# Kernel optimization log

Hardware: AMD Instinct MI355X
Metric: run time of the kernel (lower is better)

The kernel has to match this reference:

```python
import jax, jax.numpy as jnp
import numpy as np

H = 1024
B_DIM = 64  # bottleneck
EPS = 1e-5

def setup_inputs() -> dict:
    key = jax.random.key(0)
    ks = jax.random.split(key, 5)
    x = jax.random.normal(ks[0], (8, 4096, H), dtype=jnp.float32)
    norm_w = jnp.ones((H,), jnp.float32)
    norm_b = jnp.zeros((H,), jnp.float32)
    # nn.Linear default init ~ U(-1/sqrt(fan_in), 1/sqrt(fan_in))
    lim_d = 1.0 / np.sqrt(H)
    down_w = jax.random.uniform(ks[1], (B_DIM, H), jnp.float32, -lim_d, lim_d)
    down_b = jax.random.uniform(ks[2], (B_DIM,), jnp.float32, -lim_d, lim_d)
    # NOTE: original inits up to zeros; we use small random values so the
    # computation (and gradients) are non-degenerate for kernel testing.
    lim_u = 1.0 / np.sqrt(B_DIM)
    up_w = jax.random.uniform(ks[3], (H, B_DIM), jnp.float32, -lim_u, lim_u)
    up_b = jax.random.uniform(ks[4], (H,), jnp.float32, -lim_u, lim_u)
    return {"x": x, "norm_w": norm_w, "norm_b": norm_b,
            "down_w": down_w, "down_b": down_b, "up_w": up_w, "up_b": up_b}

def reference(x, norm_w, norm_b, down_w, down_b, up_w, up_b):
    # LayerNorm over last dim, eps=1e-5 (PyTorch default)
    mu = jnp.mean(x, axis=-1, keepdims=True)
    var = jnp.mean(jnp.square(x - mu), axis=-1, keepdims=True)
    xn = (x - mu) * jax.lax.rsqrt(var + EPS) * norm_w + norm_b
    # down-proj [B,S,H] @ [H,b] -> [B,S,b]
    h = jnp.einsum('bsh,dh->bsd', xn, down_w) + down_b
    h = jax.nn.gelu(h, approximate=False)  # torch nn.GELU default = exact erf
    # up-proj [B,S,b] @ [b,H] -> [B,S,H], residual add
    out = jnp.einsum('bsd,hd->bsh', h, up_w) + up_b
    return x + out
```

## Files before the change

### kernel.cpp

```cpp
#include <hip/hip_runtime.h>


#define HDIM  1024
#define BDIM  64
#define XROWB 4112

using s16x8 = __attribute__((ext_vector_type(8))) short;
using f32x4 = __attribute__((ext_vector_type(4))) float;

__device__ float g_wstat[128];

__device__ __forceinline__ short f2bf(float f) {
  unsigned u = __builtin_bit_cast(unsigned, f);
  u += 0x7fffu + ((u >> 16) & 1u);
  return (short)(u >> 16);
}
__device__ __forceinline__ float bf2f(short s) {
  unsigned u = ((unsigned)(unsigned short)s) << 16;
  return __builtin_bit_cast(float, u);
}

__device__ __forceinline__ void gload16(const void* g, void* l) {
  __builtin_amdgcn_global_load_lds(
      (const __attribute__((address_space(1))) void*)g,
      (__attribute__((address_space(3))) void*)l,
      16, 0, 0);
}

extern "C" __global__ void prep_weights(const float* __restrict__ dw,
                                        const float* __restrict__ uw,
                                        const float* __restrict__ nw,
                                        const float* __restrict__ nb,
                                        const float* __restrict__ db,
                                        short* __restrict__ wsbf) {
  const int b = blockIdx.x;
  if (b < 64) {
    int tid = b * 256 + threadIdx.x;
    if (tid < 8192) {
      int off = tid * 8;
      int k = off & (HDIM - 1);
      f32x4 v0 = *(const f32x4*)(dw + off);
      f32x4 v1 = *(const f32x4*)(dw + off + 4);
      f32x4 g0 = *(const f32x4*)(nw + k);
      f32x4 g1 = *(const f32x4*)(nw + k + 4);
      s16x8 o;
#pragma unroll
      for (int j = 0; j < 4; ++j) {
        o[j]     = f2bf(v0[j] * g0[j]);
        o[j + 4] = f2bf(v1[j] * g1[j]);
      }
      *(s16x8*)(wsbf + tid * 8) = o;
    } else {
      int off = (tid - 8192) * 8;
      f32x4 v0 = *(const f32x4*)(uw + off);
      f32x4 v1 = *(const f32x4*)(uw + off + 4);
      s16x8 o;
#pragma unroll
      for (int j = 0; j < 4; ++j) { o[j] = f2bf(v0[j]); o[j + 4] = f2bf(v1[j]); }
      *(s16x8*)(wsbf + tid * 8) = o;
    }
  } else {
    const int t = threadIdx.x;
    const int n = t >> 2, p = t & 3;
    const float* dwn = dw + n * HDIM;
    float s1 = 0.f, s2 = 0.f;
    for (int j = 0; j < 32; ++j) {
      int k = p * 256 + j * 8;
      f32x4 v0 = *(const f32x4*)(dwn + k);
      f32x4 v1 = *(const f32x4*)(dwn + k + 4);
      f32x4 g0 = *(const f32x4*)(nw + k);
      f32x4 g1 = *(const f32x4*)(nw + k + 4);
      f32x4 b0 = *(const f32x4*)(nb + k);
      f32x4 b1 = *(const f32x4*)(nb + k + 4);
#pragma unroll
      for (int jj = 0; jj < 4; ++jj) {
        s1 += bf2f(f2bf(v0[jj] * g0[jj])) + bf2f(f2bf(v1[jj] * g1[jj]));
        s2 += v0[jj] * b0[jj] + v1[jj] * b1[jj];
      }
    }
    s1 += __shfl_xor(s1, 1); s1 += __shfl_xor(s1, 2);
    s2 += __shfl_xor(s2, 1); s2 += __shfl_xor(s2, 2);
    if (p == 0) {
      g_wstat[n]      = s1;
      g_wstat[64 + n] = db[n] + s2;
    }
  }
}

extern "C" __global__ __launch_bounds__(512, 4)
void adapter_fused(const float* __restrict__ x,
                   const float* __restrict__ ub,
                   const short* __restrict__ dwb,
                   const short* __restrict__ uwb,
                   float* __restrict__ out)
{
  __shared__ __align__(16) char  xf[16 * XROWB];
  __shared__ __align__(16) float part[2][64][20];
  __shared__ __align__(16) short g[16][72];
  __shared__ float shalf[2][16];
  __shared__ float qhalf[2][16];

  const int t    = threadIdx.x;
  const int w    = t >> 6;
  const int lane = t & 63;
  const int q    = lane >> 4;
  const int c    = lane & 15;
  const size_t rowbase = (size_t)blockIdx.x * 16;

  {
    const char* gx = (const char*)(x + rowbase * HDIM);
#pragma unroll
    for (int i = 0; i < 8; ++i) {
      const int ch = w * 8 + i;
      gload16(gx + ch * 1024 + lane * 16,
              xf + (ch >> 2) * XROWB + (ch & 3) * 1024);
    }
  }
  __syncthreads();

  {
    const int kh = w >> 2, nw = w & 3;
    const char*  arow = xf + c * XROWB + kh * 2048;
    const short* pB   = dwb + (size_t)(nw * 16 + c) * HDIM + kh * 512 + q * 8;
    f32x4 acc = {0.f, 0.f, 0.f, 0.f};
    float sum = 0.f, ssq = 0.f;
#pragma unroll
    for (int ks = 0; ks < 16; ++ks) {
      f32x4 u0 = *(const f32x4*)(arow + ks * 128 + q * 32);
      f32x4 u1 = *(const f32x4*)(arow + ks * 128 + q * 32 + 16);
      s16x8 b = *(const s16x8*)(pB + ks * 32);
      s16x8 a;
#pragma unroll
      for (int j = 0; j < 4; ++j) {
        float f0 = u0[j]; sum += f0; ssq += f0 * f0; a[j]     = f2bf(f0);
        float f1 = u1[j]; sum += f1; ssq += f1 * f1; a[j + 4] = f2bf(f1);
      }
      acc = __builtin_amdgcn_mfma_f32_16x16x32_bf16(a, b, acc, 0, 0, 0);
    }
    sum += __shfl_xor(sum, 16); sum += __shfl_xor(sum, 32);
    ssq += __shfl_xor(ssq, 16); ssq += __shfl_xor(ssq, 32);
    if (nw == 0 && lane < 16) { shalf[kh][c] = sum; qhalf[kh][c] = ssq; }
    *(f32x4*)&part[kh][nw * 16 + c][q * 4] = acc;
  }
  __syncthreads();

  if (w < 4) {
    const int n = w * 16 + c;
    f32x4 p0 = *(const f32x4*)&part[0][n][q * 4];
    f32x4 p1 = *(const f32x4*)&part[1][n][q * 4];
    f32x4 h4 = p0 + p1;
    float sT = shalf[0][c] + shalf[1][c];
    float qT = qhalf[0][c] + qhalf[1][c];
    float muv = sT * (1.0f / HDIM);
    float rsv = rsqrtf(qT * (1.0f / HDIM) - muv * muv + 1e-5f);
    const float sdw = g_wstat[n];
    const float dbv = g_wstat[64 + n];
#pragma unroll
    for (int i = 0; i < 4; ++i) {
      const float m  = __shfl(muv, q * 4 + i);
      const float rv = __shfl(rsv, q * 4 + i);
      float h = rv * (h4[i] - m * sdw) + dbv;
      g[q * 4 + i][n] = f2bf(0.5f * h * (1.0f + erff(h * 0.70710678118654752f)));
    }
  }
  __syncthreads();

  {
    const s16x8 a0 = *(const s16x8*)&g[c][q * 8];
    const s16x8 a1 = *(const s16x8*)&g[c][32 + q * 8];
    const short* pu = uwb + (size_t)(w * 128 + c) * BDIM + q * 8;
    float* ob = out + rowbase * HDIM + w * 128 + c;
#pragma unroll 2
    for (int nt = 0; nt < 8; ++nt) {
      const short* uwrow = pu + (size_t)nt * 16 * BDIM;
      s16x8 b0 = *(const s16x8*)(uwrow);
      s16x8 b1 = *(const s16x8*)(uwrow + 32);
      f32x4 o4 = {0.f, 0.f, 0.f, 0.f};
      o4 = __builtin_amdgcn_mfma_f32_16x16x32_bf16(a0, b0, o4, 0, 0, 0);
      o4 = __builtin_amdgcn_mfma_f32_16x16x32_bf16(a1, b1, o4, 0, 0, 0);
      const int nc = w * 128 + nt * 16 + c;
      const float ubv = ub[nc];
#pragma unroll
      for (int i = 0; i < 4; ++i) {
        const int m = q * 4 + i;
        float res = *(const float*)(xf + m * XROWB + nc * 4);
        ob[(size_t)m * HDIM + nt * 16] = o4[i] + ubv + res;
      }
    }
  }
}

extern "C" void kernel_launch(void* const* d_in, const int* in_sizes, int n_in,
                              void* d_out, int out_size, void* d_ws, size_t ws_size,
                              hipStream_t stream) {
  const float* x  = (const float*)d_in[0];
  const float* nw = (const float*)d_in[1];
  const float* nb = (const float*)d_in[2];
  const float* dw = (const float*)d_in[3];
  const float* db = (const float*)d_in[4];
  const float* uw = (const float*)d_in[5];
  const float* ub = (const float*)d_in[6];
  float* out = (float*)d_out;

  short* wsbf = (short*)d_ws;
  prep_weights<<<65, 256, 0, stream>>>(dw, uw, nw, nb, db, wsbf);

  const int rows = in_sizes[0] / HDIM;
  const int grid = rows / 16;
  adapter_fused<<<grid, 512, 0, stream>>>(x, ub, wsbf, wsbf + 65536, out);
}
```

Before: 299.3 us.

## Make fused adapter kernel persistent over 8 row tiles with double-buffered LDS prefetch

```diff
diff --git a/kernel.cpp b/kernel.cpp
--- a/kernel.cpp
+++ b/kernel.cpp
@@ -4,6 +4,7 @@
 #define HDIM  1024
 #define BDIM  64
 #define XROWB 4112
+#define TILES 8
 
 using s16x8 = __attribute__((ext_vector_type(8))) short;
 using f32x4 = __attribute__((ext_vector_type(4))) float;
@@ -87,105 +88,146 @@
   }
 }
 
-extern "C" __global__ __launch_bounds__(512, 4)
+extern "C" __global__ __launch_bounds__(1024, 4)
 void adapter_fused(const float* __restrict__ x,
                    const float* __restrict__ ub,
                    const short* __restrict__ dwb,
                    const short* __restrict__ uwb,
                    float* __restrict__ out)
 {
-  __shared__ __align__(16) char  xf[16 * XROWB];
-  __shared__ __align__(16) float part[2][64][20];
+  __shared__ __align__(16) char  xfa[16 * XROWB];
+  __shared__ __align__(16) char  xfb[16 * XROWB];
+  __shared__ __align__(16) float part[4][64][20];
   __shared__ __align__(16) short g[16][72];
-  __shared__ float shalf[2][16];
-  __shared__ float qhalf[2][16];
-
-  const int t    = threadIdx.x;
-  const int w    = t >> 6;
-  const int lane = t & 63;
+  __shared__ float ssumS[4][16];
+  __shared__ float sssqS[4][16];
+
+  const int tid  = threadIdx.x;
+  const int w    = tid >> 6;
+  const int lane = tid & 63;
   const int q    = lane >> 4;
   const int c    = lane & 15;
-  const size_t rowbase = (size_t)blockIdx.x * 16;
-
+  const int kh   = w >> 2;
+  const int nw   = w & 3;
+  const size_t baserow = (size_t)blockIdx.x * (TILES * 16);
+
+  s16x8 bf[8];
   {
-    const char* gx = (const char*)(x + rowbase * HDIM);
-#pragma unroll
-    for (int i = 0; i < 8; ++i) {
-      const int ch = w * 8 + i;
-      gload16(gx + ch * 1024 + lane * 16,
-              xf + (ch >> 2) * XROWB + (ch & 3) * 1024);
-    }
-  }
-  __syncthreads();
-
+    const short* pB = dwb + (size_t)(nw * 16 + c) * HDIM + kh * 256 + q * 8;
+#pragma unroll
+    for (int ks = 0; ks < 8; ++ks) bf[ks] = *(const s16x8*)(pB + ks * 32);
+  }
+  s16x8 u0f[4], u1f[4]; float ubv[4];
   {
-    const int kh = w >> 2, nw = w & 3;
-    const char*  arow = xf + c * XROWB + kh * 2048;
-    const short* pB   = dwb + (size_t)(nw * 16 + c) * HDIM + kh * 512 + q * 8;
-    f32x4 acc = {0.f, 0.f, 0.f, 0.f};
-    float sum = 0.f, ssq = 0.f;
-#pragma unroll
-    for (int ks = 0; ks < 16; ++ks) {
-      f32x4 u0 = *(const f32x4*)(arow + ks * 128 + q * 32);
-      f32x4 u1 = *(const f32x4*)(arow + ks * 128 + q * 32 + 16);
-      s16x8 b = *(const s16x8*)(pB + ks * 32);
-      s16x8 a;
-#pragma unroll
-      for (int j = 0; j < 4; ++j) {
-        float f0 = u0[j]; sum += f0; ssq += f0 * f0; a[j]     = f2bf(f0);
-        float f1 = u1[j]; sum += f1; ssq += f1 * f1; a[j + 4] = f2bf(f1);
-      }
-      acc = __builtin_amdgcn_mfma_f32_16x16x32_bf16(a, b, acc, 0, 0, 0);
-    }
-    sum += __shfl_xor(sum, 16); sum += __shfl_xor(sum, 32);
-    ssq += __shfl_xor(ssq, 16); ssq += __shfl_xor(ssq, 32);
-    if (nw == 0 && lane < 16) { shalf[kh][c] = sum; qhalf[kh][c] = ssq; }
-    *(f32x4*)&part[kh][nw * 16 + c][q * 4] = acc;
-  }
-  __syncthreads();
-
-  if (w < 4) {
-    const int n = w * 16 + c;
-    f32x4 p0 = *(const f32x4*)&part[0][n][q * 4];
-    f32x4 p1 = *(const f32x4*)&part[1][n][q * 4];
-    f32x4 h4 = p0 + p1;
-    float sT = shalf[0][c] + shalf[1][c];
-    float qT = qhalf[0][c] + qhalf[1][c];
-    float muv = sT * (1.0f / HDIM);
-    float rsv = rsqrtf(qT * (1.0f / HDIM) - muv * muv + 1e-5f);
-    const float sdw = g_wstat[n];
-    const float dbv = g_wstat[64 + n];
-#pragma unroll
-    for (int i = 0; i < 4; ++i) {
-      const float m  = __shfl(muv, q * 4 + i);
-      const float rv = __shfl(rsv, q * 4 + i);
-      float h = rv * (h4[i] - m * sdw) + dbv;
-      g[q * 4 + i][n] = f2bf(0.5f * h * (1.0f + erff(h * 0.70710678118654752f)));
-    }
-  }
-  __syncthreads();
-
-  {
-    const s16x8 a0 = *(const s16x8*)&g[c][q * 8];
-    const s16x8 a1 = *(const s16x8*)&g[c][32 + q * 8];
-    const short* pu = uwb + (size_t)(w * 128 + c) * BDIM + q * 8;
-    float* ob = out + rowbase * HDIM + w * 128 + c;
-#pragma unroll 2
-    for (int nt = 0; nt < 8; ++nt) {
-      const short* uwrow = pu + (size_t)nt * 16 * BDIM;
-      s16x8 b0 = *(const s16x8*)(uwrow);
-      s16x8 b1 = *(const s16x8*)(uwrow + 32);
-      f32x4 o4 = {0.f, 0.f, 0.f, 0.f};
-      o4 = __builtin_amdgcn_mfma_f32_16x16x32_bf16(a0, b0, o4, 0, 0, 0);
-      o4 = __builtin_amdgcn_mfma_f32_16x16x32_bf16(a1, b1, o4, 0, 0, 0);
-      const int nc = w * 128 + nt * 16 + c;
-      const float ubv = ub[nc];
+    const short* pu = uwb + (size_t)(w * 64 + c) * BDIM + q * 8;
+#pragma unroll
+    for (int nt = 0; nt < 4; ++nt) {
+      u0f[nt] = *(const s16x8*)(pu + (size_t)nt * 16 * BDIM);
+      u1f[nt] = *(const s16x8*)(pu + (size_t)nt * 16 * BDIM + 32);
+      ubv[nt] = ub[w * 64 + nt * 16 + c];
+    }
+  }
+  float sdw = 0.f, dbv = 0.f;
+  if (w < 4) { sdw = g_wstat[w * 16 + c]; dbv = g_wstat[64 + w * 16 + c]; }
+
+  char* cur = xfa;
+  char* nxt = xfb;
+  auto dma_tile = [&](int tt, char* dst) {
+    const char* gx = (const char*)(x + (baserow + (size_t)tt * 16 + w) * HDIM);
+    char* ld = dst + w * XROWB;
+#pragma unroll
+    for (int i = 0; i < 4; ++i)
+      gload16(gx + i * 1024 + lane * 16, ld + i * 1024);
+  };
+
+  dma_tile(0, xfa);
+  dma_tile(1, xfb);
+  asm volatile("s_waitcnt vmcnt(4)" ::: "memory");
+  __builtin_amdgcn_s_barrier();
+  __builtin_amdgcn_sched_barrier(0);
+
+  for (int t = 0; t < TILES; ++t) {
+    const size_t trow = baserow + (size_t)t * 16;
+
+    {
+      const char* arow = cur + c * XROWB + kh * 1024;
+      f32x4 acc = {0.f, 0.f, 0.f, 0.f};
+      float sum = 0.f, ssq = 0.f;
+#pragma unroll
+      for (int ks = 0; ks < 8; ++ks) {
+        f32x4 u0 = *(const f32x4*)(arow + ks * 128 + q * 32);
+        f32x4 u1 = *(const f32x4*)(arow + ks * 128 + q * 32 + 16);
+        s16x8 a;
+#pragma unroll
+        for (int j = 0; j < 4; ++j) {
+          float f0 = u0[j]; sum += f0; ssq += f0 * f0; a[j]     = f2bf(f0);
+          float f1 = u1[j]; sum += f1; ssq += f1 * f1; a[j + 4] = f2bf(f1);
+        }
+        acc = __builtin_amdgcn_mfma_f32_16x16x32_bf16(a, bf[ks], acc, 0, 0, 0);
+      }
+      sum += __shfl_xor(sum, 16); sum += __shfl_xor(sum, 32);
+      ssq += __shfl_xor(ssq, 16); ssq += __shfl_xor(ssq, 32);
+      if (nw == 0 && lane < 16) { ssumS[kh][c] = sum; sssqS[kh][c] = ssq; }
+      *(f32x4*)&part[kh][nw * 16 + c][q * 4] = acc;
+    }
+    asm volatile("s_waitcnt lgkmcnt(0)" ::: "memory");
+    __builtin_amdgcn_s_barrier();
+    __builtin_amdgcn_sched_barrier(0);
+
+    if (w < 4) {
+      const int n = w * 16 + c;
+      f32x4 h4 = *(const f32x4*)&part[0][n][q * 4];
+      h4 += *(const f32x4*)&part[1][n][q * 4];
+      h4 += *(const f32x4*)&part[2][n][q * 4];
+      h4 += *(const f32x4*)&part[3][n][q * 4];
+      float sT = (ssumS[0][c] + ssumS[1][c]) + (ssumS[2][c] + ssumS[3][c]);
+      float qT = (sssqS[0][c] + sssqS[1][c]) + (sssqS[2][c] + sssqS[3][c]);
+      float muv = sT * (1.0f / HDIM);
+      float rsv = rsqrtf(qT * (1.0f / HDIM) - muv * muv + 1e-5f);
 #pragma unroll
       for (int i = 0; i < 4; ++i) {
-        const int m = q * 4 + i;
-        float res = *(const float*)(xf + m * XROWB + nc * 4);
-        ob[(size_t)m * HDIM + nt * 16] = o4[i] + ubv + res;
-      }
+        const float m  = __shfl(muv, q * 4 + i);
+        const float rv = __shfl(rsv, q * 4 + i);
+        float h = rv * (h4[i] - m * sdw) + dbv;
+        g[q * 4 + i][n] = f2bf(0.5f * h * (1.0f + erff(h * 0.70710678118654752f)));
+      }
+    }
+    asm volatile("s_waitcnt lgkmcnt(0)" ::: "memory");
+    __builtin_amdgcn_s_barrier();
+    __builtin_amdgcn_sched_barrier(0);
+
+    {
+      const s16x8 a0 = *(const s16x8*)&g[c][q * 8];
+      const s16x8 a1 = *(const s16x8*)&g[c][32 + q * 8];
+      float* ob = out + trow * HDIM;
+#pragma unroll
+      for (int nt = 0; nt < 4; ++nt) {
+        f32x4 o4 = {0.f, 0.f, 0.f, 0.f};
+        o4 = __builtin_amdgcn_mfma_f32_16x16x32_bf16(a0, u0f[nt], o4, 0, 0, 0);
+        o4 = __builtin_amdgcn_mfma_f32_16x16x32_bf16(a1, u1f[nt], o4, 0, 0, 0);
+        const int ncol = w * 64 + nt * 16 + c;
+#pragma unroll
+        for (int i = 0; i < 4; ++i) {
+          const int m = q * 4 + i;
+          float res = *(const float*)(cur + m * XROWB + ncol * 4);
+          ob[(size_t)m * HDIM + ncol] = o4[i] + ubv[nt] + res;
+        }
+      }
+    }
+
+    if (t + 1 < TILES) {
+      asm volatile("s_waitcnt lgkmcnt(0)" ::: "memory");
+      __builtin_amdgcn_s_barrier();
+      __builtin_amdgcn_sched_barrier(0);
+      if (t + 2 < TILES) {
+        dma_tile(t + 2, cur);
+        asm volatile("s_waitcnt vmcnt(20)" ::: "memory");
+      } else {
+        asm volatile("s_waitcnt vmcnt(16)" ::: "memory");
+      }
+      __builtin_amdgcn_s_barrier();
+      __builtin_amdgcn_sched_barrier(0);
+      char* tmp = cur; cur = nxt; nxt = tmp;
     }
   }
 }
@@ -206,6 +248,6 @@
   prep_weights<<<65, 256, 0, stream>>>(dw, uw, nw, nb, db, wsbf);
 
   const int rows = in_sizes[0] / HDIM;
-  const int grid = rows / 16;
-  adapter_fused<<<grid, 512, 0, stream>>>(x, ub, wsbf, wsbf + 65536, out);
-}
+  const int grid = rows / (16 * TILES);
+  adapter_fused<<<grid, 1024, 0, stream>>>(x, ub, wsbf, wsbf + 65536, out);
+}
```

After: 282.0 us. 1.06x faster.
